# Performance work log

Hardware: AMD Instinct MI355X
Metric: run time of the kernel (lower is better)

The kernel has to match this reference:

```python
import jax, jax.numpy as jnp
import numpy as np

B, NF, V, D, ND = 4096, 26, 100000, 64, 13
KERNELS = (7, 5, 3)
TOPKS = (23, 8, 3)  # k-max schedule derived from n=26, l=3 per CCPM formula
BN_EPS = 1e-5


def setup_inputs() -> dict:
    key = jax.random.key(0)
    ks = jax.random.split(key, 16)
    sparse = jax.random.randint(ks[0], (B, NF), 0, V)
    dense = jax.random.normal(ks[1], (B, ND), dtype=jnp.float32)
    embed_tables = jax.random.normal(ks[2], (NF, V, D), dtype=jnp.float32) * 0.01
    # conv weights OIHW, kernel (k,1)
    cw1 = jax.random.normal(ks[3], (64, 1, 7, 1), dtype=jnp.float32) * 0.1
    cb1 = jnp.zeros((64,), jnp.float32)
    cw2 = jax.random.normal(ks[4], (32, 64, 5, 1), dtype=jnp.float32) * 0.05
    cb2 = jnp.zeros((32,), jnp.float32)
    cw3 = jax.random.normal(ks[5], (16, 32, 3, 1), dtype=jnp.float32) * 0.05
    cb3 = jnp.zeros((16,), jnp.float32)
    DIN = TOPKS[-1] * 16 * D + ND  # 3*16*64+13 = 3085
    W1 = jax.random.normal(ks[6], (DIN, 256), dtype=jnp.float32) * 0.02
    b1 = jnp.zeros((256,), jnp.float32)
    g1 = jnp.ones((256,), jnp.float32)
    be1 = jnp.zeros((256,), jnp.float32)
    W2 = jax.random.normal(ks[7], (256, 128), dtype=jnp.float32) * 0.05
    b2 = jnp.zeros((128,), jnp.float32)
    g2 = jnp.ones((128,), jnp.float32)
    be2 = jnp.zeros((128,), jnp.float32)
    W3 = jax.random.normal(ks[8], (128, 1), dtype=jnp.float32) * 0.05
    b3 = jnp.zeros((1,), jnp.float32)
    return dict(sparse=sparse, dense=dense, embed_tables=embed_tables,
                cw1=cw1, cb1=cb1, cw2=cw2, cb2=cb2, cw3=cw3, cb3=cb3,
                W1=W1, b1=b1, g1=g1, be1=be1, W2=W2, b2=b2, g2=g2, be2=be2,
                W3=W3, b3=b3)


def _cnn_layer(x, w, b, k, topk):
    # ZeroPad2d pads H (feat axis) symmetrically by k//2, nothing along W.
    y = jax.lax.conv_general_dilated(
        x, w, window_strides=(1, 1), padding=[(k // 2, k // 2), (0, 0)],
        dimension_numbers=("NCHW", "OIHW", "NCHW"))
    y = jnp.tanh(y + b[None, :, None, None])
    # torch.topk along dim=2 (H), sorted descending values
    yt = jnp.swapaxes(y, 2, 3)            # [B,C,W,H]
    vals, _ = jax.lax.top_k(yt, topk)     # [B,C,W,k]
    return jnp.swapaxes(vals, 2, 3)       # [B,C,k,W]


def _bn(x, g, b):
    mu = x.mean(0)
    var = x.var(0)
    return g * (x - mu) * jax.lax.rsqrt(var + BN_EPS) + b


def reference(sparse, dense, embed_tables, cw1, cb1, cw2, cb2, cw3, cb3,
              W1, b1, g1, be1, W2, b2, g2, be2, W3, b3):
    # sparse embedding lookup per field: [B, NF, D]
    emb = embed_tables[jnp.arange(NF)[None, :], sparse]
    x = emb[:, None, :, :]  # [B,1,NF,D]
    x = _cnn_layer(x, cw1, cb1, KERNELS[0], TOPKS[0])
    x = _cnn_layer(x, cw2, cb2, KERNELS[1], TOPKS[1])
    x = _cnn_layer(x, cw3, cb3, KERNELS[2], TOPKS[2])  # [B,16,3,64]
    flat = x.reshape(x.shape[0], -1)
    h = jnp.concatenate([flat, dense], axis=1)  # [B, 3085]
    h = jnp.tanh(_bn(h @ W1 + b1, g1, be1))
    h = jnp.tanh(_bn(h @ W2 + b2, g2, be2))
    out = (h @ W3 + b3)[:, 0]  # logits, sigmoid_out=False
    return out
```

## Files before the change

### kernel.cpp

```cpp
#include <hip/hip_runtime.h>
#include <cstdint>
#include <cstddef>

#define B_SZ   4096
#define NF     26
#define VOC    100000
#define LDH    3088
#define DIN    3085

typedef __attribute__((ext_vector_type(8))) short short8;
typedef __attribute__((ext_vector_type(4))) float f32x4;

__device__ __forceinline__ float fast_tanh(float x) {
    float e = __expf(2.0f * x);
    return 1.0f - 2.0f * __builtin_amdgcn_rcpf(e + 1.0f);
}
__device__ __forceinline__ unsigned short f2bf(float x) {
    union { float f; unsigned u; } v; v.f = x;
    return (unsigned short)((v.u + 0x7FFFu + ((v.u >> 16) & 1u)) >> 16);
}
__device__ __forceinline__ unsigned short f2h(float x) {
    union { _Float16 h; unsigned short u; } v; v.h = (_Float16)x; return v.u;
}
__device__ __forceinline__ float h2f(unsigned short u) {
    union { unsigned short u; _Float16 h; } v; v.u = u; return (float)v.h;
}

template<int N>
__device__ __forceinline__ void oem_sort(float (&a)[N]) {
#pragma unroll
    for (int p = 1; p < N; p <<= 1) {
#pragma unroll
        for (int k = p; k >= 1; k >>= 1) {
#pragma unroll
            for (int j = k % p; j + k < N; j += 2 * k) {
#pragma unroll
                for (int i = 0; i < k; ++i) {
                    int lo = i + j, hi = i + j + k;
                    if (hi < N && (lo / (2 * p) == hi / (2 * p))) {
                        float x = a[lo], y = a[hi];
                        a[lo] = fminf(x, y);
                        a[hi] = fmaxf(x, y);
                    }
                }
            }
        }
    }
}

__device__ __forceinline__ void bclean8(float (&a)[8]) {
#pragma unroll
    for (int j = 4; j >= 1; j >>= 1) {
#pragma unroll
        for (int i = 0; i < 8; ++i) {
            if ((i & j) == 0 && (i | j) < 8) {
                float x = a[i], y = a[i + j];
                a[i] = fminf(x, y);
                a[i + j] = fmaxf(x, y);
            }
        }
    }
}
__device__ __forceinline__ void bclean4(float (&a)[4]) {
#pragma unroll
    for (int j = 2; j >= 1; j >>= 1) {
#pragma unroll
        for (int i = 0; i < 4; ++i) {
            if ((i & j) == 0 && (i | j) < 4) {
                float x = a[i], y = a[i + j];
                a[i] = fminf(x, y);
                a[i + j] = fmaxf(x, y);
            }
        }
    }
}

__global__ void prep_kernel(const float* __restrict__ cw1, const float* __restrict__ cw2,
                            const float* __restrict__ cw3, const float* __restrict__ dense,
                            float* __restrict__ w1t, unsigned short* __restrict__ w2b,
                            unsigned short* __restrict__ w3b, float* __restrict__ sums,
                            float* __restrict__ hmat)
{
    int idx = blockIdx.x * blockDim.x + threadIdx.x;
    if (idx < 448) {
        int c = idx / 7, j = idx % 7;
        w1t[j * 64 + c] = cw1[idx];
    } else if (idx < 10688) {
        int o = idx - 448;
        int c2 = o / 320, k = o % 320;
        int j = k >> 6, c = k & 63;
        w2b[o] = f2bf(cw2[(c2 * 64 + c) * 5 + j]);
    } else if (idx < 12224) {
        int o = idx - 10688;
        int c3 = o / 96, k = o % 96;
        int j = k >> 5, cc = k & 31;
        w3b[o] = f2bf(cw3[(c3 * 32 + cc) * 3 + j]);
    } else if (idx < 12992) {
        sums[idx - 12224] = 0.f;
    }
    int di = idx - 12992;
    if (di >= 0 && di < B_SZ * 13) {
        int b = di / 13, j = di % 13;
        hmat[(size_t)b * LDH + 3072 + j] = dense[di];
    }
}

__global__ __launch_bounds__(256, 3) void cnn_kernel(
    const int* __restrict__ sparse, const float* __restrict__ tables,
    const float* __restrict__ w1t, const float* __restrict__ cb1,
    const unsigned short* __restrict__ w2b, const float* __restrict__ cb2,
    const unsigned short* __restrict__ w3b, const float* __restrict__ cb3,
    float* __restrict__ hmat)
{
    const int d0 = blockIdx.x * 8;
    const int b  = blockIdx.y;
    const int tid = threadIdx.x;

    __shared__ __align__(16) unsigned short t1s[8 * 1800];
    __shared__ __align__(16) unsigned short y2s[8 * 32 * 25];
    __shared__ __align__(16) unsigned short t2bf[8 * 328];
    __shared__ __align__(16) float h0s[8 * 32];
    __shared__ __align__(16) float y3s[8 * 128];
    __shared__ int sidx[NF];

    if (tid < NF) sidx[tid] = sparse[b * NF + tid];
    __syncthreads();

    for (int x = tid; x < 2560; x += 256) {
        int dd = x / 320, r = x % 320;
        int i5 = r >> 6, c = r & 63;
        int i = (i5 < 2) ? i5 : (23 + i5);
        t1s[dd * 1800 + i * 64 + c] = 0;
    }
    for (int x = tid; x < 512; x += 256) {
        int dd = x >> 6, r = x & 63;
        int i = (r >> 5) * 9, cc = r & 31;
        t2bf[dd * 328 + i * 32 + cc] = 0;
    }
    if (tid < 48) {
        int dd = tid / 6, r = tid % 6;
        int i = (r < 3) ? r : (26 + r);
        h0s[dd * 32 + i] = 0.f;
    } else {
        int t = tid - 48;
        if (t < 208) {
            int fi = t >> 3, dd = t & 7;
            h0s[dd * 32 + 3 + fi] =
                tables[((size_t)fi * VOC + sidx[fi]) * 64 + d0 + dd];
        }
    }
    __syncthreads();

#pragma unroll
    for (int t = 0; t < 2; ++t) {
        int task = tid + 256 * t;
        int dd = task >> 6, c = task & 63;
        float w1r[7];
#pragma unroll
        for (int j = 0; j < 7; ++j) w1r[j] = w1t[j * 64 + c];
        float bias = cb1[c];
        float hr[32];
#pragma unroll
        for (int i = 0; i < 32; ++i) hr[i] = h0s[dd * 32 + i];
        float arr[26];
#pragma unroll
        for (int f = 0; f < 26; ++f) {
            float s = bias;
#pragma unroll
            for (int j = 0; j < 7; ++j) s += w1r[j] * hr[f + j];
            arr[f] = s;
        }
        oem_sort<26>(arr);
        unsigned short* row = &t1s[dd * 1800 + c];
#pragma unroll
        for (int r = 0; r < 23; ++r) row[(2 + r) * 64] = f2bf(fast_tanh(arr[25 - r]));
    }
    __syncthreads();

    {
        const int lane = tid & 63;
        const int w = tid >> 6;
        const int quad = lane >> 4;
        const int m = lane & 15;
        const int e = m >> 3, dd = m & 7;
        const int n = lane & 15;

        short8 Bf0[10], Bf1[10];
#pragma unroll
        for (int ks = 0; ks < 10; ++ks) {
            Bf0[ks] = *reinterpret_cast<const short8*>(w2b + (n * 320 + ks * 32 + quad * 8));
            Bf1[ks] = *reinterpret_cast<const short8*>(w2b + ((16 + n) * 320 + ks * 32 + quad * 8));
        }
        float bias0 = cb2[n], bias1 = cb2[16 + n];

#pragma unroll
        for (int pi = 0; pi < 3; ++pi) {
            int p = w + pi * 4;
            int f0 = 2 * p;
            f32x4 acc0 = {bias0, bias0, bias0, bias0};
            f32x4 acc1 = {bias1, bias1, bias1, bias1};
            const unsigned short* abase = &t1s[dd * 1800 + (f0 + e) * 64 + quad * 8];
#pragma unroll
            for (int ks = 0; ks < 10; ++ks) {
                short8 af = *reinterpret_cast<const short8*>(abase + ks * 32);
                acc0 = __builtin_amdgcn_mfma_f32_16x16x32_bf16(af, Bf0[ks], acc0, 0, 0, 0);
                acc1 = __builtin_amdgcn_mfma_f32_16x16x32_bf16(af, Bf1[ks], acc1, 0, 0, 0);
            }
#pragma unroll
            for (int r = 0; r < 4; ++r) {
                int mm = quad * 4 + r;
                int ee = mm >> 3, dw = mm & 7;
                int f = f0 + ee;
                if (f < 23) {
                    y2s[(dw * 32 + n) * 25 + f]      = f2h(acc0[r]);
                    y2s[(dw * 32 + 16 + n) * 25 + f] = f2h(acc1[r]);
                }
            }
        }
    }
    __syncthreads();

    {
        int dd = tid >> 5, c2 = tid & 31;
        const unsigned short* src = &y2s[(dd * 32 + c2) * 25];
        float va[8], vb[8], vc[7];
#pragma unroll
        for (int f = 0; f < 8; ++f) va[f] = h2f(src[f]);
#pragma unroll
        for (int f = 0; f < 8; ++f) vb[f] = h2f(src[8 + f]);
#pragma unroll
        for (int f = 0; f < 7; ++f) vc[f] = h2f(src[16 + f]);
        oem_sort<8>(va);
        oem_sort<8>(vb);
        oem_sort<7>(vc);
        float mg[8];
#pragma unroll
        for (int i = 0; i < 8; ++i) mg[i] = fmaxf(va[i], vb[7 - i]);
        bclean8(mg);
        float m2[8];
        m2[7] = mg[7];
#pragma unroll
        for (int i = 0; i < 7; ++i) m2[i] = fmaxf(mg[i], vc[6 - i]);
        bclean8(m2);
        unsigned short* row = &t2bf[dd * 328 + c2];
#pragma unroll
        for (int r = 0; r < 8; ++r) row[(1 + r) * 32] = f2bf(fast_tanh(m2[7 - r]));
    }
    __syncthreads();

    {
        const int lane = tid & 63;
        const int w = tid >> 6;
        const int quad = lane >> 4;
        const int m = lane & 15;
        const int e = m >> 3, dd = m & 7;
        const int n = lane & 15;
        int f0 = 2 * w;

        f32x4 acc;
        float bias = cb3[n];
        acc[0] = bias; acc[1] = bias; acc[2] = bias; acc[3] = bias;
        const unsigned short* abase = &t2bf[dd * 328 + (f0 + e) * 32 + quad * 8];
#pragma unroll
        for (int ks = 0; ks < 3; ++ks) {
            short8 af = *reinterpret_cast<const short8*>(abase + ks * 32);
            short8 bf = *reinterpret_cast<const short8*>(w3b + (n * 96 + ks * 32 + quad * 8));
            acc = __builtin_amdgcn_mfma_f32_16x16x32_bf16(af, bf, acc, 0, 0, 0);
        }
#pragma unroll
        for (int r = 0; r < 4; ++r) {
            int mm = quad * 4 + r;
            int ee = mm >> 3, dw = mm & 7;
            int f = f0 + ee;
            y3s[dw * 128 + n * 8 + f] = acc[r];
        }
    }
    __syncthreads();

    if (tid < 128) {
        int dd = tid >> 4, c3 = tid & 15;
        const float* yb = &y3s[dd * 128 + c3 * 8];
        float a4[4], b4[4];
#pragma unroll
        for (int f = 0; f < 4; ++f) { a4[f] = yb[f]; b4[f] = yb[4 + f]; }
        oem_sort<4>(a4);
        oem_sort<4>(b4);
        float mg[4];
#pragma unroll
        for (int i = 0; i < 4; ++i) mg[i] = fmaxf(a4[i], b4[3 - i]);
        bclean4(mg);
        float* orow = &hmat[(size_t)b * LDH + c3 * 192 + d0 + dd];
        orow[0]   = fast_tanh(mg[3]);
        orow[64]  = fast_tanh(mg[2]);
        orow[128] = fast_tanh(mg[1]);
    }
}

template<bool APPLY>
__global__ __launch_bounds__(256) void gemm_kernel(
    const float* __restrict__ A, int lda, int K,
    const float* __restrict__ Bm, int ldb,
    const float* __restrict__ scl, const float* __restrict__ sft,
    float* __restrict__ C, int N)
{
    __shared__ __align__(16) float As[16 * 36];
    __shared__ __align__(16) float Bs[16 * 68];
    const int tid = threadIdx.x;
    const int row0 = blockIdx.y * 32;
    const int n0 = blockIdx.x * 64;
    const int ty = tid >> 4, tx = tid & 15;

    float acc[2][4];
#pragma unroll
    for (int i = 0; i < 2; ++i)
#pragma unroll
        for (int j = 0; j < 4; ++j) acc[i][j] = 0.f;

    const int kk_a = tid & 15, rb_a = tid >> 4;
    const int kr_b = tid >> 4, nb_b = (tid & 15) * 4;

    for (int k0 = 0; k0 < K; k0 += 16) {
        __syncthreads();
        {
            int k = k0 + kk_a;
            bool ok = (k < K);
            float sc = 0.f, sh = 0.f;
            if (APPLY && ok) { sc = scl[k]; sh = sft[k]; }
#pragma unroll
            for (int p = 0; p < 2; ++p) {
                int r = rb_a + p * 16;
                float v = 0.f;
                if (ok) {
                    v = A[(size_t)(row0 + r) * lda + k];
                    if (APPLY) v = fast_tanh(v * sc + sh);
                }
                As[kk_a * 36 + r] = v;
            }
        }
        {
            int k = k0 + kr_b;
            float4 bv = make_float4(0.f, 0.f, 0.f, 0.f);
            if (k < K) bv = *reinterpret_cast<const float4*>(&Bm[(size_t)k * ldb + n0 + nb_b]);
            *reinterpret_cast<float4*>(&Bs[kr_b * 68 + nb_b]) = bv;
        }
        __syncthreads();
#pragma unroll
        for (int kk = 0; kk < 16; ++kk) {
            float2 av = *reinterpret_cast<const float2*>(&As[kk * 36 + ty * 2]);
            float4 bv = *reinterpret_cast<const float4*>(&Bs[kk * 68 + tx * 4]);
            float bb[4] = {bv.x, bv.y, bv.z, bv.w};
#pragma unroll
            for (int j = 0; j < 4; ++j) {
                acc[0][j] += av.x * bb[j];
                acc[1][j] += av.y * bb[j];
            }
        }
    }

#pragma unroll
    for (int i = 0; i < 2; ++i) {
        float4 ov = make_float4(acc[i][0], acc[i][1], acc[i][2], acc[i][3]);
        *reinterpret_cast<float4*>(&C[(size_t)(row0 + ty * 2 + i) * N + n0 + tx * 4]) = ov;
    }
}

__global__ void bnstats_kernel(const float* __restrict__ z, int ncols,
                               float* __restrict__ sums, float* __restrict__ sumsq)
{
    int col = threadIdx.x;
    int r0 = blockIdx.x * 16;
    float s = 0.f, q = 0.f;
#pragma unroll
    for (int i = 0; i < 16; ++i) {
        float v = z[(size_t)(r0 + i) * ncols + col];
        s += v; q += v * v;
    }
    atomicAdd(&sums[col], s);
    atomicAdd(&sumsq[col], q);
}

__global__ void bnfin_kernel(const float* __restrict__ sums, const float* __restrict__ sumsq,
                             const float* __restrict__ g, const float* __restrict__ be,
                             int ncols, float* __restrict__ scl, float* __restrict__ sft)
{
    int i = threadIdx.x + blockIdx.x * blockDim.x;
    if (i < ncols) {
        float mu = sums[i] * (1.0f / 4096.0f);
        float var = sumsq[i] * (1.0f / 4096.0f) - mu * mu;
        float s = g[i] * rsqrtf(var + 1e-5f);
        scl[i] = s;
        sft[i] = be[i] - mu * s;
    }
}

__global__ __launch_bounds__(256) void final_kernel(
    const float* __restrict__ z2, const float* __restrict__ scl, const float* __restrict__ sft,
    const float* __restrict__ W3, const float* __restrict__ b3, float* __restrict__ out)
{
    int lane = threadIdx.x & 63;
    int wv = threadIdx.x >> 6;
    int r = blockIdx.x * 4 + wv;
    float p = 0.f;
#pragma unroll
    for (int t = 0; t < 2; ++t) {
        int n = lane + t * 64;
        p += fast_tanh(z2[(size_t)r * 128 + n] * scl[n] + sft[n]) * W3[n];
    }
#pragma unroll
    for (int off = 32; off > 0; off >>= 1) p += __shfl_down(p, off);
    if (lane == 0) out[r] = p + b3[0];
}

extern "C" void kernel_launch(void* const* d_in, const int* in_sizes, int n_in,
                              void* d_out, int out_size, void* d_ws, size_t ws_size,
                              hipStream_t stream) {
    const int*   sparse = (const int*)  d_in[0];
    const float* dense  = (const float*)d_in[1];
    const float* tables = (const float*)d_in[2];
    const float* cw1    = (const float*)d_in[3];
    const float* cb1    = (const float*)d_in[4];
    const float* cw2    = (const float*)d_in[5];
    const float* cb2    = (const float*)d_in[6];
    const float* cw3    = (const float*)d_in[7];
    const float* cb3    = (const float*)d_in[8];
    const float* W1     = (const float*)d_in[9];
    const float* g1     = (const float*)d_in[11];
    const float* be1    = (const float*)d_in[12];
    const float* W2     = (const float*)d_in[13];
    const float* g2     = (const float*)d_in[15];
    const float* be2    = (const float*)d_in[16];
    const float* W3     = (const float*)d_in[17];
    const float* b3     = (const float*)d_in[18];
    float* out = (float*)d_out;

    float* ws   = (float*)d_ws;
    float* hmat = ws;
    float* z1   = hmat + (size_t)B_SZ * LDH;
    float* z2   = z1 + (size_t)B_SZ * 256;
    float* w1t  = z2 + (size_t)B_SZ * 128;
    unsigned short* w2b = (unsigned short*)(w1t + 448);
    unsigned short* w3b = (unsigned short*)(w1t + 448 + 5120);
    float* sums = w1t + 448 + 5120 + 768;
    float* a1   = sums + 768;
    float* c1   = a1 + 256;
    float* a2   = c1 + 256;
    float* c2v  = a2 + 128;

    prep_kernel<<<259, 256, 0, stream>>>(cw1, cw2, cw3, dense, w1t, w2b, w3b, sums, hmat);

    cnn_kernel<<<dim3(8, B_SZ), 256, 0, stream>>>(sparse, tables, w1t, cb1,
                                                  w2b, cb2, w3b, cb3, hmat);

    gemm_kernel<false><<<dim3(4, 128), 256, 0, stream>>>(hmat, LDH, DIN, W1, 256,
                                                         nullptr, nullptr, z1, 256);
    bnstats_kernel<<<256, 256, 0, stream>>>(z1, 256, sums, sums + 256);
    bnfin_kernel<<<1, 256, 0, stream>>>(sums, sums + 256, g1, be1, 256, a1, c1);

    gemm_kernel<true><<<dim3(2, 128), 256, 0, stream>>>(z1, 256, 256, W2, 128,
                                                        a1, c1, z2, 128);
    bnstats_kernel<<<256, 128, 0, stream>>>(z2, 128, sums + 512, sums + 640);
    bnfin_kernel<<<1, 128, 0, stream>>>(sums + 512, sums + 640, g2, be2, 128, a2, c2v);

    final_kernel<<<1024, 256, 0, stream>>>(z2, a2, c2v, W3, b3, out);
}
```

Before: 1.569 ms.

## Fuse BN stats into GEMM epilogues, prefetch GEMM tiles, widen CNN blocks to 512

The CNN kernel now runs 512 threads per block so each thread handles a single conv1 channel task, with guards for the later stages that use fewer threads. The GEMM kernel gains register prefetch of the next A/B tile and an epilogue that reduces column sums and sums of squares in shared memory before issuing atomics. This removes the separate bnstats and bnfin kernels, since BN scale and shift are now computed inside the next GEMM and the final kernel. The change cuts kernel launches and a re-read of z1/z2, at the cost of more register and shared-memory pressure and idle threads in parts of the CNN kernel.

```diff
diff --git a/kernel.cpp b/kernel.cpp
--- a/kernel.cpp
+++ b/kernel.cpp
@@ -105,7 +105,7 @@
     }
 }
 
-__global__ __launch_bounds__(256, 3) void cnn_kernel(
+__global__ __launch_bounds__(512, 6) void cnn_kernel(
     const int* __restrict__ sparse, const float* __restrict__ tables,
     const float* __restrict__ w1t, const float* __restrict__ cb1,
     const unsigned short* __restrict__ w2b, const float* __restrict__ cb2,
@@ -126,14 +126,14 @@
     if (tid < NF) sidx[tid] = sparse[b * NF + tid];
     __syncthreads();
 
-    for (int x = tid; x < 2560; x += 256) {
+    for (int x = tid; x < 2560; x += 512) {
         int dd = x / 320, r = x % 320;
         int i5 = r >> 6, c = r & 63;
         int i = (i5 < 2) ? i5 : (23 + i5);
         t1s[dd * 1800 + i * 64 + c] = 0;
     }
-    for (int x = tid; x < 512; x += 256) {
-        int dd = x >> 6, r = x & 63;
+    {
+        int dd = tid >> 6, r = tid & 63;
         int i = (r >> 5) * 9, cc = r & 31;
         t2bf[dd * 328 + i * 32 + cc] = 0;
     }
@@ -141,20 +141,16 @@
         int dd = tid / 6, r = tid % 6;
         int i = (r < 3) ? r : (26 + r);
         h0s[dd * 32 + i] = 0.f;
-    } else {
+    } else if (tid < 256) {
         int t = tid - 48;
-        if (t < 208) {
-            int fi = t >> 3, dd = t & 7;
-            h0s[dd * 32 + 3 + fi] =
-                tables[((size_t)fi * VOC + sidx[fi]) * 64 + d0 + dd];
-        }
-    }
-    __syncthreads();
-
-#pragma unroll
-    for (int t = 0; t < 2; ++t) {
-        int task = tid + 256 * t;
-        int dd = task >> 6, c = task & 63;
+        int fi = t >> 3, dd = t & 7;
+        h0s[dd * 32 + 3 + fi] =
+            tables[((size_t)fi * VOC + sidx[fi]) * 64 + d0 + dd];
+    }
+    __syncthreads();
+
+    {
+        int dd = tid >> 6, c = tid & 63;
         float w1r[7];
 #pragma unroll
         for (int j = 0; j < 7; ++j) w1r[j] = w1t[j * 64 + c];
@@ -194,33 +190,35 @@
         float bias0 = cb2[n], bias1 = cb2[16 + n];
 
 #pragma unroll
-        for (int pi = 0; pi < 3; ++pi) {
-            int p = w + pi * 4;
-            int f0 = 2 * p;
-            f32x4 acc0 = {bias0, bias0, bias0, bias0};
-            f32x4 acc1 = {bias1, bias1, bias1, bias1};
-            const unsigned short* abase = &t1s[dd * 1800 + (f0 + e) * 64 + quad * 8];
-#pragma unroll
-            for (int ks = 0; ks < 10; ++ks) {
-                short8 af = *reinterpret_cast<const short8*>(abase + ks * 32);
-                acc0 = __builtin_amdgcn_mfma_f32_16x16x32_bf16(af, Bf0[ks], acc0, 0, 0, 0);
-                acc1 = __builtin_amdgcn_mfma_f32_16x16x32_bf16(af, Bf1[ks], acc1, 0, 0, 0);
-            }
-#pragma unroll
-            for (int r = 0; r < 4; ++r) {
-                int mm = quad * 4 + r;
-                int ee = mm >> 3, dw = mm & 7;
-                int f = f0 + ee;
-                if (f < 23) {
-                    y2s[(dw * 32 + n) * 25 + f]      = f2h(acc0[r]);
-                    y2s[(dw * 32 + 16 + n) * 25 + f] = f2h(acc1[r]);
+        for (int pi = 0; pi < 2; ++pi) {
+            int p = w + pi * 8;
+            if (p < 12) {
+                int f0 = 2 * p;
+                f32x4 acc0 = {bias0, bias0, bias0, bias0};
+                f32x4 acc1 = {bias1, bias1, bias1, bias1};
+                const unsigned short* abase = &t1s[dd * 1800 + (f0 + e) * 64 + quad * 8];
+#pragma unroll
+                for (int ks = 0; ks < 10; ++ks) {
+                    short8 af = *reinterpret_cast<const short8*>(abase + ks * 32);
+                    acc0 = __builtin_amdgcn_mfma_f32_16x16x32_bf16(af, Bf0[ks], acc0, 0, 0, 0);
+                    acc1 = __builtin_amdgcn_mfma_f32_16x16x32_bf16(af, Bf1[ks], acc1, 0, 0, 0);
                 }
-            }
-        }
-    }
-    __syncthreads();
-
-    {
+#pragma unroll
+                for (int r = 0; r < 4; ++r) {
+                    int mm = quad * 4 + r;
+                    int ee = mm >> 3, dw = mm & 7;
+                    int f = f0 + ee;
+                    if (f < 23) {
+                        y2s[(dw * 32 + n) * 25 + f]      = f2h(acc0[r]);
+                        y2s[(dw * 32 + 16 + n) * 25 + f] = f2h(acc1[r]);
+                    }
+                }
+            }
+        }
+    }
+    __syncthreads();
+
+    if (tid < 256) {
         int dd = tid >> 5, c2 = tid & 31;
         const unsigned short* src = &y2s[(dd * 32 + c2) * 25];
         float va[8], vb[8], vc[7];
@@ -251,28 +249,30 @@
     {
         const int lane = tid & 63;
         const int w = tid >> 6;
-        const int quad = lane >> 4;
-        const int m = lane & 15;
-        const int e = m >> 3, dd = m & 7;
-        const int n = lane & 15;
-        int f0 = 2 * w;
-
-        f32x4 acc;
-        float bias = cb3[n];
-        acc[0] = bias; acc[1] = bias; acc[2] = bias; acc[3] = bias;
-        const unsigned short* abase = &t2bf[dd * 328 + (f0 + e) * 32 + quad * 8];
-#pragma unroll
-        for (int ks = 0; ks < 3; ++ks) {
-            short8 af = *reinterpret_cast<const short8*>(abase + ks * 32);
-            short8 bf = *reinterpret_cast<const short8*>(w3b + (n * 96 + ks * 32 + quad * 8));
-            acc = __builtin_amdgcn_mfma_f32_16x16x32_bf16(af, bf, acc, 0, 0, 0);
-        }
-#pragma unroll
-        for (int r = 0; r < 4; ++r) {
-            int mm = quad * 4 + r;
-            int ee = mm >> 3, dw = mm & 7;
-            int f = f0 + ee;
-            y3s[dw * 128 + n * 8 + f] = acc[r];
+        if (w < 4) {
+            const int quad = lane >> 4;
+            const int m = lane & 15;
+            const int e = m >> 3, dd = m & 7;
+            const int n = lane & 15;
+            int f0 = 2 * w;
+
+            f32x4 acc;
+            float bias = cb3[n];
+            acc[0] = bias; acc[1] = bias; acc[2] = bias; acc[3] = bias;
+            const unsigned short* abase = &t2bf[dd * 328 + (f0 + e) * 32 + quad * 8];
+#pragma unroll
+            for (int ks = 0; ks < 3; ++ks) {
+                short8 af = *reinterpret_cast<const short8*>(abase + ks * 32);
+                short8 bf = *reinterpret_cast<const short8*>(w3b + (n * 96 + ks * 32 + quad * 8));
+                acc = __builtin_amdgcn_mfma_f32_16x16x32_bf16(af, bf, acc, 0, 0, 0);
+            }
+#pragma unroll
+            for (int r = 0; r < 4; ++r) {
+                int mm = quad * 4 + r;
+                int ee = mm >> 3, dw = mm & 7;
+                int f = f0 + ee;
+                y3s[dw * 128 + n * 8 + f] = acc[r];
+            }
         }
     }
     __syncthreads();
@@ -296,20 +296,33 @@
     }
 }
 
-template<bool APPLY>
+template<bool APPLY, bool STATS>
 __global__ __launch_bounds__(256) void gemm_kernel(
     const float* __restrict__ A, int lda, int K,
     const float* __restrict__ Bm, int ldb,
-    const float* __restrict__ scl, const float* __restrict__ sft,
-    float* __restrict__ C, int N)
+    const float* __restrict__ bns, const float* __restrict__ bnq,
+    const float* __restrict__ g, const float* __restrict__ be,
+    float* __restrict__ C, int N,
+    float* __restrict__ osum, float* __restrict__ osumsq)
 {
     __shared__ __align__(16) float As[16 * 36];
     __shared__ __align__(16) float Bs[16 * 68];
+    __shared__ float scl_s[256], sft_s[256];
+    __shared__ float red[16 * 64];
     const int tid = threadIdx.x;
     const int row0 = blockIdx.y * 32;
     const int n0 = blockIdx.x * 64;
     const int ty = tid >> 4, tx = tid & 15;
 
+    if (APPLY) {
+        float mu = bns[tid] * (1.0f / 4096.0f);
+        float var = bnq[tid] * (1.0f / 4096.0f) - mu * mu;
+        float s = g[tid] * rsqrtf(var + 1e-5f);
+        scl_s[tid] = s;
+        sft_s[tid] = be[tid] - mu * s;
+        __syncthreads();
+    }
+
     float acc[2][4];
 #pragma unroll
     for (int i = 0; i < 2; ++i)
@@ -319,31 +332,37 @@
     const int kk_a = tid & 15, rb_a = tid >> 4;
     const int kr_b = tid >> 4, nb_b = (tid & 15) * 4;
 
+    float a_r[2];
+    float4 b_r;
+    {
+        int k = kk_a;
+#pragma unroll
+        for (int p = 0; p < 2; ++p)
+            a_r[p] = A[(size_t)(row0 + rb_a + p * 16) * lda + k];
+        b_r = *reinterpret_cast<const float4*>(&Bm[(size_t)kr_b * ldb + n0 + nb_b]);
+    }
+
     for (int k0 = 0; k0 < K; k0 += 16) {
-        __syncthreads();
         {
-            int k = k0 + kk_a;
+#pragma unroll
+            for (int p = 0; p < 2; ++p) {
+                float v = a_r[p];
+                if (APPLY) { int k = k0 + kk_a; v = fast_tanh(v * scl_s[k] + sft_s[k]); }
+                As[kk_a * 36 + rb_a + p * 16] = v;
+            }
+            *reinterpret_cast<float4*>(&Bs[kr_b * 68 + nb_b]) = b_r;
+        }
+        __syncthreads();
+        if (k0 + 16 < K) {
+            int k = k0 + 16 + kk_a;
             bool ok = (k < K);
-            float sc = 0.f, sh = 0.f;
-            if (APPLY && ok) { sc = scl[k]; sh = sft[k]; }
-#pragma unroll
-            for (int p = 0; p < 2; ++p) {
-                int r = rb_a + p * 16;
-                float v = 0.f;
-                if (ok) {
-                    v = A[(size_t)(row0 + r) * lda + k];
-                    if (APPLY) v = fast_tanh(v * sc + sh);
-                }
-                As[kk_a * 36 + r] = v;
-            }
-        }
-        {
-            int k = k0 + kr_b;
-            float4 bv = make_float4(0.f, 0.f, 0.f, 0.f);
-            if (k < K) bv = *reinterpret_cast<const float4*>(&Bm[(size_t)k * ldb + n0 + nb_b]);
-            *reinterpret_cast<float4*>(&Bs[kr_b * 68 + nb_b]) = bv;
-        }
-        __syncthreads();
+#pragma unroll
+            for (int p = 0; p < 2; ++p)
+                a_r[p] = ok ? A[(size_t)(row0 + rb_a + p * 16) * lda + k] : 0.f;
+            int kb = k0 + 16 + kr_b;
+            b_r = (kb < K) ? *reinterpret_cast<const float4*>(&Bm[(size_t)kb * ldb + n0 + nb_b])
+                           : make_float4(0.f, 0.f, 0.f, 0.f);
+        }
 #pragma unroll
         for (int kk = 0; kk < 16; ++kk) {
             float2 av = *reinterpret_cast<const float2*>(&As[kk * 36 + ty * 2]);
@@ -355,6 +374,7 @@
                 acc[1][j] += av.y * bb[j];
             }
         }
+        __syncthreads();
     }
 
 #pragma unroll
@@ -362,39 +382,34 @@
         float4 ov = make_float4(acc[i][0], acc[i][1], acc[i][2], acc[i][3]);
         *reinterpret_cast<float4*>(&C[(size_t)(row0 + ty * 2 + i) * N + n0 + tx * 4]) = ov;
     }
-}
-
-__global__ void bnstats_kernel(const float* __restrict__ z, int ncols,
-                               float* __restrict__ sums, float* __restrict__ sumsq)
-{
-    int col = threadIdx.x;
-    int r0 = blockIdx.x * 16;
-    float s = 0.f, q = 0.f;
-#pragma unroll
-    for (int i = 0; i < 16; ++i) {
-        float v = z[(size_t)(r0 + i) * ncols + col];
-        s += v; q += v * v;
-    }
-    atomicAdd(&sums[col], s);
-    atomicAdd(&sumsq[col], q);
-}
-
-__global__ void bnfin_kernel(const float* __restrict__ sums, const float* __restrict__ sumsq,
-                             const float* __restrict__ g, const float* __restrict__ be,
-                             int ncols, float* __restrict__ scl, float* __restrict__ sft)
-{
-    int i = threadIdx.x + blockIdx.x * blockDim.x;
-    if (i < ncols) {
-        float mu = sums[i] * (1.0f / 4096.0f);
-        float var = sumsq[i] * (1.0f / 4096.0f) - mu * mu;
-        float s = g[i] * rsqrtf(var + 1e-5f);
-        scl[i] = s;
-        sft[i] = be[i] - mu * s;
+
+    if (STATS) {
+#pragma unroll
+        for (int j = 0; j < 4; ++j) red[ty * 64 + tx * 4 + j] = acc[0][j] + acc[1][j];
+        __syncthreads();
+        if (tid < 64) {
+            float s = 0.f;
+#pragma unroll
+            for (int t = 0; t < 16; ++t) s += red[t * 64 + tid];
+            atomicAdd(&osum[n0 + tid], s);
+        }
+        __syncthreads();
+#pragma unroll
+        for (int j = 0; j < 4; ++j)
+            red[ty * 64 + tx * 4 + j] = acc[0][j] * acc[0][j] + acc[1][j] * acc[1][j];
+        __syncthreads();
+        if (tid < 64) {
+            float q = 0.f;
+#pragma unroll
+            for (int t = 0; t < 16; ++t) q += red[t * 64 + tid];
+            atomicAdd(&osumsq[n0 + tid], q);
+        }
     }
 }
 
 __global__ __launch_bounds__(256) void final_kernel(
-    const float* __restrict__ z2, const float* __restrict__ scl, const float* __restrict__ sft,
+    const float* __restrict__ z2, const float* __restrict__ bns, const float* __restrict__ bnq,
+    const float* __restrict__ g, const float* __restrict__ be,
     const float* __restrict__ W3, const float* __restrict__ b3, float* __restrict__ out)
 {
     int lane = threadIdx.x & 63;
@@ -404,7 +419,11 @@
 #pragma unroll
     for (int t = 0; t < 2; ++t) {
         int n = lane + t * 64;
-        p += fast_tanh(z2[(size_t)r * 128 + n] * scl[n] + sft[n]) * W3[n];
+        float mu = bns[n] * (1.0f / 4096.0f);
+        float var = bnq[n] * (1.0f / 4096.0f) - mu * mu;
+        float s = g[n] * rsqrtf(var + 1e-5f);
+        float sft = be[n] - mu * s;
+        p += fast_tanh(z2[(size_t)r * 128 + n] * s + sft) * W3[n];
     }
 #pragma unroll
     for (int off = 32; off > 0; off >>= 1) p += __shfl_down(p, off);
@@ -441,25 +460,21 @@
     unsigned short* w2b = (unsigned short*)(w1t + 448);
     unsigned short* w3b = (unsigned short*)(w1t + 448 + 5120);
     float* sums = w1t + 448 + 5120 + 768;
-    float* a1   = sums + 768;
-    float* c1   = a1 + 256;
-    float* a2   = c1 + 256;
-    float* c2v  = a2 + 128;
 
     prep_kernel<<<259, 256, 0, stream>>>(cw1, cw2, cw3, dense, w1t, w2b, w3b, sums, hmat);
 
-    cnn_kernel<<<dim3(8, B_SZ), 256, 0, stream>>>(sparse, tables, w1t, cb1,
+    cnn_kernel<<<dim3(8, B_SZ), 512, 0, stream>>>(sparse, tables, w1t, cb1,
                                                   w2b, cb2, w3b, cb3, hmat);
 
-    gemm_kernel<false><<<dim3(4, 128), 256, 0, stream>>>(hmat, LDH, DIN, W1, 256,
-                                                         nullptr, nullptr, z1, 256);
-    bnstats_kernel<<<256, 256, 0, stream>>>(z1, 256, sums, sums + 256);
-    bnfin_kernel<<<1, 256, 0, stream>>>(sums, sums + 256, g1, be1, 256, a1, c1);
-
-    gemm_kernel<true><<<dim3(2, 128), 256, 0, stream>>>(z1, 256, 256, W2, 128,
-                                                        a1, c1, z2, 128);
-    bnstats_kernel<<<256, 128, 0, stream>>>(z2, 128, sums + 512, sums + 640);
-    bnfin_kernel<<<1, 128, 0, stream>>>(sums + 512, sums + 640, g2, be2, 128, a2, c2v);
-
-    final_kernel<<<1024, 256, 0, stream>>>(z2, a2, c2v, W3, b3, out);
-}
+    gemm_kernel<false, true><<<dim3(4, 128), 256, 0, stream>>>(
+        hmat, LDH, DIN, W1, 256,
+        nullptr, nullptr, nullptr, nullptr,
+        z1, 256, sums, sums + 256);
+
+    gemm_kernel<true, true><<<dim3(2, 128), 256, 0, stream>>>(
+        z1, 256, 256, W2, 128,
+        sums, sums + 256, g1, be1,
+        z2, 128, sums + 512, sums + 640);
+
+    final_kernel<<<1024, 256, 0, stream>>>(z2, sums + 512, sums + 640, g2, be2, W3, b3, out);
+}
```

Measured after the change: 2.127 ms. 35.6% more time.
